# Performance work log

Measured on AMD Instinct MI355X. Metric: run time of the kernel, lower is better.

## Reference

```python
import jax, jax.numpy as jnp
import numpy as np

NUM_USERS = 4096
NUM_ITEMS = 8192
EMBED_DIM = 64
NUM_LAYERS = 3


def setup_inputs() -> dict:
    key = jax.random.key(0)
    k1, k2 = jax.random.split(key)
    # embedding table for users+items (nn.Embedding init normal std=0.1)
    x = jax.random.normal(k1, (NUM_USERS + NUM_ITEMS, EMBED_DIM), dtype=jnp.float32) * 0.1
    # dense 0/1 user-item interaction matrix (forward applies torch.nonzero to it)
    edge_index = jax.random.randint(k2, (NUM_USERS, NUM_ITEMS), 0, 2, dtype=jnp.int32)
    return {"x": x, "edge_index": edge_index}


def reference(x, edge_index):
    U, I, L = NUM_USERS, NUM_ITEMS, NUM_LAYERS
    adj = edge_index.astype(jnp.float32)  # [U, I], 0/1
    # symmetric degree normalization: adj / sqrt(deg_u * deg_i), nan (0/0) -> 0
    deg_u = jnp.sum(adj, axis=1)  # [U]
    deg_i = jnp.sum(adj, axis=0)  # [I]
    denom = jnp.sqrt(deg_u[:, None] * deg_i[None, :])  # [U, I]
    weights = jnp.where(denom > 0, adj / jnp.where(denom > 0, denom, 1.0), 0.0)
    # weights is identical every layer (depends only on edge_index)
    acc = jnp.zeros_like(x)
    for _ in range(L):
        # NOTE: original code concatenates (item-side, user-side) in this order
        x = jnp.concatenate([weights.T @ x[:U], weights @ x[U:]], axis=0)  # [I+U, d]
        acc = acc + x
    # alpha = 1/(1+L) * ones applied to every layer output
    return acc / (1.0 + L)
```

## Files before the change

### kernel.cpp

```cpp
#include <hip/hip_runtime.h>

#define NU 4096
#define NI 8192
#define ND 64
#define NTOT 12288
#define CT 8
#define CB 16

typedef unsigned short u16;
typedef unsigned int u32;
typedef unsigned long long u64;

__device__ __forceinline__ u16 f2bf(float f) {
    union { float f; u32 u; } v; v.f = f;
    u32 u = v.u;
    u += 0x7FFFu + ((u >> 16) & 1u);
    return (u16)(u >> 16);
}

typedef short frag8 __attribute__((ext_vector_type(8)));
typedef float f32x4 __attribute__((ext_vector_type(4)));

__global__ __launch_bounds__(256) void k_pack2(const int* __restrict__ edge,
        u64* __restrict__ Apk, u64* __restrict__ ATpk) {
    __shared__ __align__(16) u16 At[256][40];
    __shared__ __align__(16) u64 Tt[512][6];
    const int t = threadIdx.x;
    const int u0 = (blockIdx.x >> 4) * 256;
    const int i0 = (blockIdx.x & 15) * 512;
    const int cg = t & 31;
    const int rb = t >> 5;

    #pragma unroll 4
    for (int rr = 0; rr < 32; rr++) {
        const int row = rb * 32 + rr;
        const int4* p = (const int4*)(edge + (size_t)(u0 + row) * NI + i0 + cg * 16);
        u32 bits = 0;
        #pragma unroll
        for (int m = 0; m < 4; m++) {
            int4 v = p[m];
            bits |= (v.x != 0 ? 1u : 0u) << (m * 4 + 0);
            bits |= (v.y != 0 ? 1u : 0u) << (m * 4 + 1);
            bits |= (v.z != 0 ? 1u : 0u) << (m * 4 + 2);
            bits |= (v.w != 0 ? 1u : 0u) << (m * 4 + 3);
        }
        At[row][cg] = (u16)bits;
    }
    __syncthreads();

    {
        u64* dst = Apk + (size_t)(u0 + t) * 128 + (i0 >> 6);
        #pragma unroll
        for (int q = 0; q < 4; q++) {
            uint4 v = *(const uint4*)&At[t][q * 8];
            *(uint4*)(dst + q * 2) = v;
        }
    }

    {
        const int lane = t & 63, w = t >> 6;
        const u64 M[6] = {0x00000000FFFFFFFFULL, 0x0000FFFF0000FFFFULL,
                          0x00FF00FF00FF00FFULL, 0x0F0F0F0F0F0F0F0FULL,
                          0x3333333333333333ULL, 0x5555555555555555ULL};
        #pragma unroll
        for (int sc = 0; sc < 8; sc++) {
            u64 x = *(const u64*)&At[w * 64 + lane][sc * 4];
            #pragma unroll
            for (int si = 0; si < 6; si++) {
                const int s = 32 >> si;
                u64 y = __shfl_xor(x, s, 64);
                x = (lane & s) ? ((x & ~M[si]) | ((y >> s) & M[si]))
                               : ((x &  M[si]) | ((y << s) & ~M[si]));
            }
            Tt[sc * 64 + lane][w] = x;
        }
    }
    __syncthreads();
    #pragma unroll
    for (int j = 0; j < 2; j++) {
        const int item = t * 2 + j;
        ulonglong2 a = *(const ulonglong2*)&Tt[item][0];
        ulonglong2 b = *(const ulonglong2*)&Tt[item][2];
        u64* dst = ATpk + (size_t)(i0 + item) * 64 + (u0 >> 6);
        *(ulonglong2*)dst = a;
        *(ulonglong2*)(dst + 2) = b;
    }
}

__global__ __launch_bounds__(256) void k_scale0(const float* __restrict__ x,
        const u64* __restrict__ Apk, const u64* __restrict__ ATpk,
        float* __restrict__ dsu, float* __restrict__ dsi,
        u16* __restrict__ BuT, u16* __restrict__ BiT) {
    __shared__ float sc[64];
    const int t = threadIdx.x;
    const int r0 = blockIdx.x * 64;
    {
        const int rl = t >> 2, part = t & 3;
        int cnt = 0;
        if (r0 < NU) {
            const u64* p = Apk + (size_t)(r0 + rl) * 128 + part * 32;
            #pragma unroll
            for (int i = 0; i < 32; i++) cnt += (int)__popcll(p[i]);
        } else {
            const u64* p = ATpk + (size_t)(r0 - NU + rl) * 64 + part * 16;
            #pragma unroll
            for (int i = 0; i < 16; i++) cnt += (int)__popcll(p[i]);
        }
        cnt += __shfl_xor(cnt, 1, 64);
        cnt += __shfl_xor(cnt, 2, 64);
        if (part == 0) {
            float s = cnt > 0 ? rsqrtf((float)cnt) : 0.f;
            sc[rl] = s;
            if (r0 < NU) dsu[r0 + rl] = s; else dsi[r0 - NU + rl] = s;
        }
    }
    __syncthreads();
    const int r4 = t >> 4, c4 = t & 15;
    float y[4][4];
    #pragma unroll
    for (int j = 0; j < 4; j++) {
        const int rl = r4 * 4 + j;
        const float s = sc[rl];
        float4 xv = *(const float4*)(x + (size_t)(r0 + rl) * ND + c4 * 4);
        y[j][0] = xv.x * s; y[j][1] = xv.y * s;
        y[j][2] = xv.z * s; y[j][3] = xv.w * s;
    }
    u16* dst; size_t stride; int col0;
    if (r0 < NU) { dst = BuT; stride = NU; col0 = r0; }
    else         { dst = BiT; stride = NI; col0 = r0 - NU; }
    #pragma unroll
    for (int k = 0; k < 4; k++) {
        ushort4 w;
        w.x = f2bf(y[0][k]); w.y = f2bf(y[1][k]);
        w.z = f2bf(y[2][k]); w.w = f2bf(y[3][k]);
        *(ushort4*)(dst + (size_t)(c4 * 4 + k) * stride + col0 + r4 * 4) = w;
    }
}

__global__ __launch_bounds__(256) void k_gemm(
        const u64* __restrict__ Apk, const u64* __restrict__ ATpk,
        const u16* __restrict__ BuT, const u16* __restrict__ BiT,
        float* __restrict__ Ptop, float* __restrict__ Pbot) {
    __shared__ __align__(16) u16 Bs[64][512];
    const int t = threadIdx.x, bx = blockIdx.x;
    const int lane = t & 63, w = t >> 6, lr = lane & 15, lg = lane >> 4;
    const u64* arow; const u16* dense; int Kstr, wpr, kbase; float* Pout;
    if (bx < 1024) {
        const int tile = bx >> 3, chunk = bx & 7;
        arow = ATpk + (size_t)(tile * 64) * 64 + chunk * 8; wpr = 64;
        dense = BuT; Kstr = NU; kbase = chunk * 512;
        Pout = Ptop + ((size_t)chunk * NI + tile * 64) * ND;
    } else {
        const int b2 = bx - 1024, tile = b2 >> 4, chunk = b2 & 15;
        arow = Apk + (size_t)(tile * 64) * 128 + chunk * 8; wpr = 128;
        dense = BiT; Kstr = NI; kbase = chunk * 512;
        Pout = Pbot + ((size_t)chunk * NU + tile * 64) * ND;
    }
    const u64* myrow = arow + (size_t)(w * 16 + lr) * wpr;
    u64 aw[8];
    #pragma unroll
    for (int qq = 0; qq < 4; qq++) {
        ulonglong2 v = *(const ulonglong2*)(myrow + qq * 2);
        aw[qq * 2] = v.x; aw[qq * 2 + 1] = v.y;
    }
    const u16* gsrc = dense + kbase;
    #pragma unroll
    for (int it = 0; it < 16; it++) {
        const int idx = t + it * 256;
        const int e = idx >> 6, seg = idx & 63;
        const int kk = seg >> 3, s8 = seg & 7;
        *(uint4*)&Bs[e][kk * 64 + ((s8 ^ (e & 7)) * 8)] =
            *(const uint4*)(gsrc + (size_t)e * Kstr + seg * 8);
    }
    f32x4 acc[4];
    #pragma unroll
    for (int i = 0; i < 4; i++) acc[i] = f32x4{0.f, 0.f, 0.f, 0.f};
    __syncthreads();

    #pragma unroll
    for (int kk = 0; kk < 8; kk++) {
        const u32 lo = (u32)aw[kk], hi = (u32)(aw[kk] >> 32);
        const u32 byte0 = (lo >> (lg * 8)) & 0xFFu;
        const u32 byte1 = (hi >> (lg * 8)) & 0xFFu;
        frag8 bf0, bf1;
        #pragma unroll
        for (int j = 0; j < 8; j++) {
            bf0[j] = (short)(((byte0 >> j) & 1u) ? 0x3F80 : 0);
            bf1[j] = (short)(((byte1 >> j) & 1u) ? 0x3F80 : 0);
        }
        #pragma unroll
        for (int nt = 0; nt < 4; nt++) {
            const int e = nt * 16 + lr, sw = e & 7;
            frag8 a0 = *(const frag8*)&Bs[e][kk * 64 + ((lg ^ sw) * 8)];
            frag8 a1 = *(const frag8*)&Bs[e][kk * 64 + (((4 + lg) ^ sw) * 8)];
            acc[nt] = __builtin_amdgcn_mfma_f32_16x16x32_bf16(a0, bf0, acc[nt], 0, 0, 0);
            acc[nt] = __builtin_amdgcn_mfma_f32_16x16x32_bf16(a1, bf1, acc[nt], 0, 0, 0);
        }
    }
    #pragma unroll
    for (int nt = 0; nt < 4; nt++)
        *(f32x4*)&Pout[(size_t)(w * 16 + lr) * ND + nt * 16 + lg * 4] = acc[nt];
}

__global__ __launch_bounds__(256) void k_reduce(
        const float* __restrict__ Ptop, const float* __restrict__ Pbot,
        const float* __restrict__ dsu, const float* __restrict__ dsi,
        float* __restrict__ accbuf, u16* __restrict__ BuTn,
        u16* __restrict__ BiTn, float* __restrict__ out, int layer) {
    __shared__ u16 TB[64][24];
    const int t = threadIdx.x, bx = blockIdx.x;
    const int rl = t >> 4, e4 = t & 15;
    int grow; float so;
    float sx = 0.f, sy = 0.f, sz = 0.f, sw = 0.f;
    if (bx < 512) {
        grow = bx * 16 + rl;
        const float* p = Ptop + (size_t)grow * ND + e4 * 4;
        #pragma unroll
        for (int c = 0; c < CT; c++) {
            float4 v = *(const float4*)(p + (size_t)c * NI * ND);
            sx += v.x; sy += v.y; sz += v.z; sw += v.w;
        }
        so = dsi[grow];
    } else {
        const int u = (bx - 512) * 16 + rl;
        grow = NI + u;
        const float* p = Pbot + (size_t)u * ND + e4 * 4;
        #pragma unroll
        for (int c = 0; c < CB; c++) {
            float4 v = *(const float4*)(p + (size_t)c * NU * ND);
            sx += v.x; sy += v.y; sz += v.z; sw += v.w;
        }
        so = dsu[grow - NI];
    }
    float4 y;
    y.x = sx * so; y.y = sy * so; y.z = sz * so; y.w = sw * so;
    const size_t o = (size_t)grow * ND + e4 * 4;
    if (layer == 0) {
        *(float4*)(accbuf + o) = y;
    } else if (layer == 1) {
        float4 a = *(const float4*)(accbuf + o);
        a.x += y.x; a.y += y.y; a.z += y.z; a.w += y.w;
        *(float4*)(accbuf + o) = a;
    } else {
        float4 a = *(const float4*)(accbuf + o);
        a.x = (a.x + y.x) * 0.25f; a.y = (a.y + y.y) * 0.25f;
        a.z = (a.z + y.z) * 0.25f; a.w = (a.w + y.w) * 0.25f;
        *(float4*)(out + o) = a;
    }
    if (layer != 2) {
        const float fn = (grow < NU) ? dsu[grow] : dsi[grow - NU];
        TB[e4 * 4 + 0][rl] = f2bf(y.x * fn);
        TB[e4 * 4 + 1][rl] = f2bf(y.y * fn);
        TB[e4 * 4 + 2][rl] = f2bf(y.z * fn);
        TB[e4 * 4 + 3][rl] = f2bf(y.w * fn);
        __syncthreads();
        if (t < 128) {
            const int e = t >> 1, h = t & 1;
            u16* dst; size_t stride; int col0;
            if (bx < 256)      { dst = BuTn; stride = NU; col0 = bx * 16; }
            else if (bx < 512) { dst = BiTn; stride = NI; col0 = bx * 16 - NU; }
            else               { dst = BiTn; stride = NI; col0 = (bx - 512) * 16 + NI - NU; }
            uint4 v = *(const uint4*)&TB[e][h * 8];
            *(uint4*)(dst + (size_t)e * stride + col0 + h * 8) = v;
        }
    }
}

extern "C" void kernel_launch(void* const* d_in, const int* in_sizes, int n_in,
                              void* d_out, int out_size, void* d_ws, size_t ws_size,
                              hipStream_t stream) {
    (void)in_sizes; (void)n_in; (void)out_size; (void)ws_size;
    const float* x    = (const float*)d_in[0];
    const int*   edge = (const int*)d_in[1];
    float* out = (float*)d_out;

    char* ws = (char*)d_ws;
    size_t off = 0;
    u64* Apk  = (u64*)(ws + off); off += (size_t)NU * (NI / 64) * 8;
    u64* ATpk = (u64*)(ws + off); off += (size_t)NI * (NU / 64) * 8;
    float* dsu = (float*)(ws + off); off += (size_t)NU * 4;
    float* dsi = (float*)(ws + off); off += (size_t)NI * 4;
    u16* BuT0 = (u16*)(ws + off); off += (size_t)ND * NU * 2;
    u16* BuT1 = (u16*)(ws + off); off += (size_t)ND * NU * 2;
    u16* BiT0 = (u16*)(ws + off); off += (size_t)ND * NI * 2;
    u16* BiT1 = (u16*)(ws + off); off += (size_t)ND * NI * 2;
    float* acc  = (float*)(ws + off); off += (size_t)NTOT * ND * 4;
    float* Ptop = (float*)(ws + off); off += (size_t)CT * NI * ND * 4;
    float* Pbot = (float*)(ws + off); off += (size_t)CB * NU * ND * 4;

    k_pack2<<<256, 256, 0, stream>>>(edge, Apk, ATpk);
    k_scale0<<<NTOT / 64, 256, 0, stream>>>(x, Apk, ATpk, dsu, dsi, BuT0, BiT0);

    k_gemm<<<2048, 256, 0, stream>>>(Apk, ATpk, BuT0, BiT0, Ptop, Pbot);
    k_reduce<<<768, 256, 0, stream>>>(Ptop, Pbot, dsu, dsi, acc, BuT1, BiT1, out, 0);
    k_gemm<<<2048, 256, 0, stream>>>(Apk, ATpk, BuT1, BiT1, Ptop, Pbot);
    k_reduce<<<768, 256, 0, stream>>>(Ptop, Pbot, dsu, dsi, acc, BuT0, BiT0, out, 1);
    k_gemm<<<2048, 256, 0, stream>>>(Apk, ATpk, BuT0, BiT0, Ptop, Pbot);
    k_reduce<<<768, 256, 0, stream>>>(Ptop, Pbot, dsu, dsi, acc,
                                      (u16*)nullptr, (u16*)nullptr, out, 2);
}
```

Before: 293.7 us.

## Load GEMM B tile directly into LDS and interleave chunk partials by row

The GEMM now fills its dense B tile with global_load_lds (direct global-to-LDS copies). It uses padded LDS rows instead of the XOR swizzle, which removes the register round-trip on the staging path. The partial-sum buffers change from chunk-major to row-major with chunks interleaved, and results are staged through a skewed LDS layout so stores stay coalesced. k_reduce then reads each row's chunk partials contiguously instead of striding across large planes. The trade-off is an extra LDS staging pass and two barriers at the end of the GEMM, plus reliance on correct wait ordering for the async LDS loads.

```diff
diff --git a/kernel.cpp b/kernel.cpp
--- a/kernel.cpp
+++ b/kernel.cpp
@@ -6,6 +6,7 @@
 #define NTOT 12288
 #define CT 8
 #define CB 16
+#define BROW 520
 
 typedef unsigned short u16;
 typedef unsigned int u32;
@@ -141,20 +142,30 @@
         const u64* __restrict__ Apk, const u64* __restrict__ ATpk,
         const u16* __restrict__ BuT, const u16* __restrict__ BiT,
         float* __restrict__ Ptop, float* __restrict__ Pbot) {
-    __shared__ __align__(16) u16 Bs[64][512];
+    __shared__ __align__(16) u16 Bs[64 * BROW];
     const int t = threadIdx.x, bx = blockIdx.x;
     const int lane = t & 63, w = t >> 6, lr = lane & 15, lg = lane >> 4;
-    const u64* arow; const u16* dense; int Kstr, wpr, kbase; float* Pout;
+    const u64* arow; const u16* dense; int Kstr, wpr, kbase, pstr; float* Pout;
     if (bx < 1024) {
         const int tile = bx >> 3, chunk = bx & 7;
         arow = ATpk + (size_t)(tile * 64) * 64 + chunk * 8; wpr = 64;
-        dense = BuT; Kstr = NU; kbase = chunk * 512;
-        Pout = Ptop + ((size_t)chunk * NI + tile * 64) * ND;
+        dense = BuT; Kstr = NU; kbase = chunk * 512; pstr = CT * 64;
+        Pout = Ptop + (size_t)(tile * 64) * pstr + chunk * 64;
     } else {
         const int b2 = bx - 1024, tile = b2 >> 4, chunk = b2 & 15;
         arow = Apk + (size_t)(tile * 64) * 128 + chunk * 8; wpr = 128;
-        dense = BiT; Kstr = NI; kbase = chunk * 512;
-        Pout = Pbot + ((size_t)chunk * NU + tile * 64) * ND;
+        dense = BiT; Kstr = NI; kbase = chunk * 512; pstr = CB * 64;
+        Pout = Pbot + (size_t)(tile * 64) * pstr + chunk * 64;
+    }
+    const u16* gsrc = dense + kbase;
+    #pragma unroll
+    for (int it = 0; it < 16; it++) {
+        const int e = it * 4 + w;
+        __builtin_amdgcn_global_load_lds(
+            (const __attribute__((address_space(1))) void*)
+                (gsrc + (size_t)e * Kstr + lane * 8),
+            (__attribute__((address_space(3))) void*)(&Bs[e * BROW]),
+            16, 0, 0);
     }
     const u64* myrow = arow + (size_t)(w * 16 + lr) * wpr;
     u64 aw[8];
@@ -162,15 +173,6 @@
     for (int qq = 0; qq < 4; qq++) {
         ulonglong2 v = *(const ulonglong2*)(myrow + qq * 2);
         aw[qq * 2] = v.x; aw[qq * 2 + 1] = v.y;
-    }
-    const u16* gsrc = dense + kbase;
-    #pragma unroll
-    for (int it = 0; it < 16; it++) {
-        const int idx = t + it * 256;
-        const int e = idx >> 6, seg = idx & 63;
-        const int kk = seg >> 3, s8 = seg & 7;
-        *(uint4*)&Bs[e][kk * 64 + ((s8 ^ (e & 7)) * 8)] =
-            *(const uint4*)(gsrc + (size_t)e * Kstr + seg * 8);
     }
     f32x4 acc[4];
     #pragma unroll
@@ -190,16 +192,28 @@
         }
         #pragma unroll
         for (int nt = 0; nt < 4; nt++) {
-            const int e = nt * 16 + lr, sw = e & 7;
-            frag8 a0 = *(const frag8*)&Bs[e][kk * 64 + ((lg ^ sw) * 8)];
-            frag8 a1 = *(const frag8*)&Bs[e][kk * 64 + (((4 + lg) ^ sw) * 8)];
+            const int e = nt * 16 + lr;
+            frag8 a0 = *(const frag8*)&Bs[e * BROW + kk * 64 + lg * 8];
+            frag8 a1 = *(const frag8*)&Bs[e * BROW + kk * 64 + 32 + lg * 8];
             acc[nt] = __builtin_amdgcn_mfma_f32_16x16x32_bf16(a0, bf0, acc[nt], 0, 0, 0);
             acc[nt] = __builtin_amdgcn_mfma_f32_16x16x32_bf16(a1, bf1, acc[nt], 0, 0, 0);
         }
     }
-    #pragma unroll
-    for (int nt = 0; nt < 4; nt++)
-        *(f32x4*)&Pout[(size_t)(w * 16 + lr) * ND + nt * 16 + lg * 4] = acc[nt];
+    __syncthreads();
+    float* Fs = (float*)Bs;
+    #pragma unroll
+    for (int nt = 0; nt < 4; nt++) {
+        const int row = w * 16 + lr, g = nt * 4 + lg;
+        *(f32x4*)&Fs[row * 64 + (((g + row) & 15) * 4)] = acc[nt];
+    }
+    __syncthreads();
+    #pragma unroll
+    for (int ii = 0; ii < 4; ii++) {
+        const int slot = t + ii * 256;
+        const int row = slot >> 4, g = slot & 15;
+        f32x4 v = *(const f32x4*)&Fs[row * 64 + (((g + row) & 15) * 4)];
+        *(f32x4*)&Pout[(size_t)row * pstr + g * 4] = v;
+    }
 }
 
 __global__ __launch_bounds__(256) void k_reduce(
@@ -214,20 +228,20 @@
     float sx = 0.f, sy = 0.f, sz = 0.f, sw = 0.f;
     if (bx < 512) {
         grow = bx * 16 + rl;
-        const float* p = Ptop + (size_t)grow * ND + e4 * 4;
+        const float* p = Ptop + (size_t)grow * (CT * 64) + e4 * 4;
         #pragma unroll
         for (int c = 0; c < CT; c++) {
-            float4 v = *(const float4*)(p + (size_t)c * NI * ND);
+            float4 v = *(const float4*)(p + c * 64);
             sx += v.x; sy += v.y; sz += v.z; sw += v.w;
         }
         so = dsi[grow];
     } else {
         const int u = (bx - 512) * 16 + rl;
         grow = NI + u;
-        const float* p = Pbot + (size_t)u * ND + e4 * 4;
+        const float* p = Pbot + (size_t)u * (CB * 64) + e4 * 4;
         #pragma unroll
         for (int c = 0; c < CB; c++) {
-            float4 v = *(const float4*)(p + (size_t)c * NU * ND);
+            float4 v = *(const float4*)(p + c * 64);
             sx += v.x; sy += v.y; sz += v.z; sw += v.w;
         }
         so = dsu[grow - NI];
@@ -285,8 +299,8 @@
     u16* BiT0 = (u16*)(ws + off); off += (size_t)ND * NI * 2;
     u16* BiT1 = (u16*)(ws + off); off += (size_t)ND * NI * 2;
     float* acc  = (float*)(ws + off); off += (size_t)NTOT * ND * 4;
-    float* Ptop = (float*)(ws + off); off += (size_t)CT * NI * ND * 4;
-    float* Pbot = (float*)(ws + off); off += (size_t)CB * NU * ND * 4;
+    float* Ptop = (float*)(ws + off); off += (size_t)NI * CT * 64 * 4;
+    float* Pbot = (float*)(ws + off); off += (size_t)NU * CB * 64 * 4;
 
     k_pack2<<<256, 256, 0, stream>>>(edge, Apk, ATpk);
     k_scale0<<<NTOT / 64, 256, 0, stream>>>(x, Apk, ATpk, dsu, dsi, BuT0, BiT0);
```

Measured after the change: 287.9 us. No clear change (-2.0%).
